# Optimization experiments

Hardware: AMD Instinct MI355X
Metric: run time of the kernel (lower is better)

## Reference

```python
import jax, jax.numpy as jnp
import numpy as np

N = 50000          # nodes
E = 800000         # edges
D_IN = 96          # node_encoding_length
D = 128            # hidden_encoding_length (args.node_encoding)
B = 512            # graphs in batch
MPNN_STEPS = 4
S2S_STEPS = 3


def setup_inputs() -> dict:
    key = jax.random.key(0)
    ks = jax.random.split(key, 12)
    x = jax.random.normal(ks[0], (N, D_IN), dtype=jnp.float32)
    edge_index = jax.random.randint(ks[1], (2, E), 0, N, dtype=jnp.int64)
    batch = jnp.sort(jax.random.randint(ks[2], (N,), 0, B, dtype=jnp.int64))
    s_in = 1.0 / np.sqrt(D_IN)
    W_in = jax.random.uniform(ks[3], (D, D_IN), jnp.float32, -s_in, s_in)
    b_in = jax.random.uniform(ks[4], (D,), jnp.float32, -s_in, s_in)
    s_l = 1.0 / np.sqrt(D)
    W_ih = jax.random.uniform(ks[5], (4 * D, 2 * D), jnp.float32, -s_l, s_l)
    W_hh = jax.random.uniform(ks[6], (4 * D, D), jnp.float32, -s_l, s_l)
    b_ih = jax.random.uniform(ks[7], (4 * D,), jnp.float32, -s_l, s_l)
    b_hh = jax.random.uniform(ks[8], (4 * D,), jnp.float32, -s_l, s_l)
    s_p = 1.0 / np.sqrt(2 * D)
    W_pred = jax.random.uniform(ks[9], (1, 2 * D), jnp.float32, -s_p, s_p)
    b_pred = jax.random.uniform(ks[10], (1,), jnp.float32, -s_p, s_p)
    return {"x": x, "edge_index": edge_index, "batch": batch,
            "W_in": W_in, "b_in": b_in, "W_ih": W_ih, "W_hh": W_hh,
            "b_ih": b_ih, "b_hh": b_hh, "W_pred": W_pred, "b_pred": b_pred}


def _forward(x, edge_index, batch, W_in, b_in, W_ih, W_hh, b_ih, b_hh, W_pred, b_pred):
    # input layer + relu
    h = jax.nn.relu(x @ W_in.T + b_in)                      # [N, D]
    src, dst = edge_index[0], edge_index[1]
    # precompute in-degree for mean aggregation (clamped to 1 like scatter-mean)
    deg = jax.ops.segment_sum(jnp.ones((E,), h.dtype), dst, num_segments=N)
    deg = jnp.maximum(deg, 1.0)[:, None]                    # [N, 1]
    # MPNN: gather x_j at src, mean-aggregate at dst, update x=(x+msg)/2
    for _ in range(MPNN_STEPS):
        msg = jax.ops.segment_sum(h[src], dst, num_segments=N) / deg
        h = (h + msg) * 0.5
    # Set2Set readout
    d = h.shape[1]
    q_star = jnp.zeros((B, 2 * d), h.dtype)
    hh = jnp.zeros((B, d), h.dtype)
    cc = jnp.zeros((B, d), h.dtype)
    for _ in range(S2S_STEPS):
        gates = q_star @ W_ih.T + b_ih + hh @ W_hh.T + b_hh  # [B, 4d]
        i_g, f_g, g_g, o_g = jnp.split(gates, 4, axis=-1)
        cc = jax.nn.sigmoid(f_g) * cc + jax.nn.sigmoid(i_g) * jnp.tanh(g_g)
        hh = jax.nn.sigmoid(o_g) * jnp.tanh(cc)
        q = hh                                               # [B, d]
        e = jnp.sum(h * q[batch], axis=-1)                   # [N]
        e_max = jax.ops.segment_max(e, batch, num_segments=B)
        a = jnp.exp(e - e_max[batch])
        a_sum = jax.ops.segment_sum(a, batch, num_segments=B)
        a = a / (a_sum[batch] + 1e-16)
        r = jax.ops.segment_sum(a[:, None] * h, batch, num_segments=B)  # [B, d]
        q_star = jnp.concatenate([q, r], axis=-1)
    return q_star @ W_pred.T + b_pred                        # [B, 1]


def reference(x, edge_index, batch, W_in, b_in, W_ih, W_hh, b_ih, b_hh, W_pred, b_pred):
    return _forward(x, edge_index, batch, W_in, b_in, W_ih, W_hh, b_ih, b_hh, W_pred, b_pred)
```

## Files before the change

kernel.cpp:

```cpp
#include <hip/hip_runtime.h>
#include <math.h>
#include <float.h>

#define N_NODES 50000
#define N_EDGES 800000
#define D_INP   96
#define D_HID   128
#define N_B     512
#define CAP     64
#define XS_LD   100

typedef __attribute__((ext_vector_type(4))) _Float16 half4;

__global__ void k_prep(const float* __restrict__ W_in,
                       const float* __restrict__ W_ih,
                       const float* __restrict__ W_hh,
                       float* __restrict__ Wt_in,
                       float* __restrict__ Wt2,
                       int* __restrict__ cnt) {
    int idx = blockIdx.x * 256 + threadIdx.x;
    if (idx < N_NODES) cnt[idx] = 0;
    if (idx < D_INP * D_HID) {
        int k = idx / D_HID, d = idx % D_HID;
        Wt_in[idx] = W_in[d * D_INP + k];
    }
    if (idx < 256 * 512) {
        int k = idx / 512, g = idx % 512;
        float v = W_ih[g * 256 + k];
        if (k < 128) v += W_hh[g * 128 + k];
        Wt2[idx] = v;
    }
}

__global__ void k_bucket(const int* __restrict__ src, const int* __restrict__ dst,
                         const int* __restrict__ batch,
                         int* __restrict__ cnt, int* __restrict__ esrc,
                         int* __restrict__ seg_ptr) {
    int e = blockIdx.x * 256 + threadIdx.x;
    if (e < N_EDGES) {
        int d = dst[e];
        int p = atomicAdd(&cnt[d], 1);
        if (p < CAP) esrc[d * CAP + p] = src[e];
    }
    if (e < N_NODES) {
        int n = e;
        int bc = batch[n];
        int bp = (n == 0) ? -1 : batch[n - 1];
        for (int b = bp + 1; b <= bc; b++) seg_ptr[b] = n;
        if (n == N_NODES - 1)
            for (int b = bc + 1; b <= N_B; b++) seg_ptr[b] = N_NODES;
    }
}

__global__ __launch_bounds__(256) void k_ingemm(const float* __restrict__ x,
                                                const float* __restrict__ Wt_in,
                                                const float* __restrict__ b_in,
                                                float* __restrict__ h,
                                                _Float16* __restrict__ h16) {
    __shared__ __align__(16) float xs[64 * XS_LD];
    __shared__ __align__(16) float ws[96 * 64];
    int n0 = blockIdx.x * 64;
    int d0 = blockIdx.y * 64;
    int tid = threadIdx.x;
    for (int j = tid; j < 64 * 96 / 4; j += 256) {
        int row = (j * 4) / 96, col = (j * 4) % 96;
        int node = n0 + row;
        float4 v = make_float4(0.f, 0.f, 0.f, 0.f);
        if (node < N_NODES) v = *(const float4*)&x[(size_t)node * 96 + col];
        *(float4*)&xs[row * XS_LD + col] = v;
    }
    for (int j = tid; j < 96 * 64 / 4; j += 256) {
        int k = (j * 4) / 64, dd = (j * 4) % 64;
        *(float4*)&ws[j * 4] = *(const float4*)&Wt_in[k * D_HID + d0 + dd];
    }
    __syncthreads();
    int tn = tid / 16;
    int td = tid % 16;
    float acc[4][4] = {};
    for (int k0 = 0; k0 < 96; k0 += 4) {
        float4 w0 = *(float4*)&ws[(k0 + 0) * 64 + td * 4];
        float4 w1 = *(float4*)&ws[(k0 + 1) * 64 + td * 4];
        float4 w2 = *(float4*)&ws[(k0 + 2) * 64 + td * 4];
        float4 w3 = *(float4*)&ws[(k0 + 3) * 64 + td * 4];
#pragma unroll
        for (int j = 0; j < 4; j++) {
            float4 xv = *(float4*)&xs[(tn * 4 + j) * XS_LD + k0];
            acc[j][0] += xv.x * w0.x + xv.y * w1.x + xv.z * w2.x + xv.w * w3.x;
            acc[j][1] += xv.x * w0.y + xv.y * w1.y + xv.z * w2.y + xv.w * w3.y;
            acc[j][2] += xv.x * w0.z + xv.y * w1.z + xv.z * w2.z + xv.w * w3.z;
            acc[j][3] += xv.x * w0.w + xv.y * w1.w + xv.z * w2.w + xv.w * w3.w;
        }
    }
    float4 bb = *(const float4*)&b_in[d0 + td * 4];
#pragma unroll
    for (int j = 0; j < 4; j++) {
        int node = n0 + tn * 4 + j;
        if (node < N_NODES) {
            float4 o;
            o.x = fmaxf(acc[j][0] + bb.x, 0.f);
            o.y = fmaxf(acc[j][1] + bb.y, 0.f);
            o.z = fmaxf(acc[j][2] + bb.z, 0.f);
            o.w = fmaxf(acc[j][3] + bb.w, 0.f);
            *(float4*)&h[(size_t)node * D_HID + d0 + td * 4] = o;
            half4 s;
            s.x = (_Float16)o.x; s.y = (_Float16)o.y;
            s.z = (_Float16)o.z; s.w = (_Float16)o.w;
            *(half4*)&h16[(size_t)node * D_HID + d0 + td * 4] = s;
        }
    }
}

template <bool WRITE16>
__global__ __launch_bounds__(256) void k_mpnn(const float* __restrict__ hin,
                                              const _Float16* __restrict__ hin16,
                                              float* __restrict__ hout,
                                              _Float16* __restrict__ hout16,
                                              const int* __restrict__ cnt,
                                              const int* __restrict__ esrc) {
    int g = threadIdx.x >> 5;
    int l = threadIdx.x & 31;
    int n = blockIdx.x * 8 + g;
    if (n >= N_NODES) return;
    int deg = cnt[n];
    int len = min(deg, CAP);
    const int* row = &esrc[n * CAP];
    float4 a0 = {0,0,0,0}, a1 = {0,0,0,0}, a2 = {0,0,0,0}, a3 = {0,0,0,0};
    int i = 0;
    for (; i + 4 <= len; i += 4) {
        int e0 = row[i + 0];
        int e1 = row[i + 1];
        int e2 = row[i + 2];
        int e3 = row[i + 3];
        half4 v0 = *(const half4*)&hin16[(size_t)e0 * 128 + l * 4];
        half4 v1 = *(const half4*)&hin16[(size_t)e1 * 128 + l * 4];
        half4 v2 = *(const half4*)&hin16[(size_t)e2 * 128 + l * 4];
        half4 v3 = *(const half4*)&hin16[(size_t)e3 * 128 + l * 4];
        a0.x += (float)v0.x; a0.y += (float)v0.y; a0.z += (float)v0.z; a0.w += (float)v0.w;
        a1.x += (float)v1.x; a1.y += (float)v1.y; a1.z += (float)v1.z; a1.w += (float)v1.w;
        a2.x += (float)v2.x; a2.y += (float)v2.y; a2.z += (float)v2.z; a2.w += (float)v2.w;
        a3.x += (float)v3.x; a3.y += (float)v3.y; a3.z += (float)v3.z; a3.w += (float)v3.w;
    }
    for (; i < len; i++) {
        int e0 = row[i];
        half4 v0 = *(const half4*)&hin16[(size_t)e0 * 128 + l * 4];
        a0.x += (float)v0.x; a0.y += (float)v0.y; a0.z += (float)v0.z; a0.w += (float)v0.w;
    }
    a0.x += a1.x + a2.x + a3.x;
    a0.y += a1.y + a2.y + a3.y;
    a0.z += a1.z + a2.z + a3.z;
    a0.w += a1.w + a2.w + a3.w;
    float invd = 1.0f / (float)max(deg, 1);
    float4 hv = *(const float4*)&hin[(size_t)n * 128 + l * 4];
    float4 o;
    o.x = (hv.x + a0.x * invd) * 0.5f;
    o.y = (hv.y + a0.y * invd) * 0.5f;
    o.z = (hv.z + a0.z * invd) * 0.5f;
    o.w = (hv.w + a0.w * invd) * 0.5f;
    *(float4*)&hout[(size_t)n * 128 + l * 4] = o;
    if (WRITE16) {
        half4 s;
        s.x = (_Float16)o.x; s.y = (_Float16)o.y;
        s.z = (_Float16)o.z; s.w = (_Float16)o.w;
        *(half4*)&hout16[(size_t)n * 128 + l * 4] = s;
    }
}

__device__ __forceinline__ float sigmoidf_(float v) { return 1.0f / (1.0f + expf(-v)); }

__global__ __launch_bounds__(1024) void k_s2s2(const float* __restrict__ Wt2,
                                               const float* __restrict__ b_ih,
                                               const float* __restrict__ b_hh,
                                               const float* __restrict__ h,
                                               const int* __restrict__ seg_ptr,
                                               const float* __restrict__ W_pred,
                                               const float* __restrict__ b_pred,
                                               float* __restrict__ out) {
    __shared__ __align__(16) float in_s[2 * 256];
    __shared__ __align__(16) float c_s[2 * 128];
    __shared__ __align__(16) float gates_s[2 * 512];
    __shared__ __align__(16) float gpart_s[2][2][512];
    __shared__ float smax_s[2][16];
    __shared__ float ssum_s[2][16];
    __shared__ __align__(16) float sr_s[2][16][128];

    int t = threadIdx.x;
    if (t < 512) in_s[t] = 0.f;
    if (t < 256) c_s[t] = 0.f;

    int gate = t & 511;
    int kh   = t >> 9;
    int row  = t >> 9;
    int loc  = t & 511;
    int gq   = loc >> 5;
    int l    = t & 31;
    int b    = blockIdx.x * 2 + row;
    int s0 = seg_ptr[b], s1 = seg_ptr[b + 1];

    for (int step = 0; step < 3; step++) {
        __syncthreads();
        {
            float acc0 = 0.f, acc1 = 0.f;
            int k0 = kh * 128;
#pragma unroll 8
            for (int k = k0; k < k0 + 128; k++) {
                float w = Wt2[k * 512 + gate];
                acc0 += in_s[k] * w;
                acc1 += in_s[256 + k] * w;
            }
            gpart_s[kh][0][gate] = acc0;
            gpart_s[kh][1][gate] = acc1;
        }
        __syncthreads();
        if (t < 512) {
            float bia = b_ih[t] + b_hh[t];
            gates_s[t]       = gpart_s[0][0][t] + gpart_s[1][0][t] + bia;
            gates_s[512 + t] = gpart_s[0][1][t] + gpart_s[1][1][t] + bia;
        }
        __syncthreads();
        if (t < 256) {
            int r2 = t >> 7, ff = t & 127;
            float ig = gates_s[r2 * 512 + ff];
            float fg = gates_s[r2 * 512 + 128 + ff];
            float gg = gates_s[r2 * 512 + 256 + ff];
            float og = gates_s[r2 * 512 + 384 + ff];
            float c = sigmoidf_(fg) * c_s[r2 * 128 + ff] + sigmoidf_(ig) * tanhf(gg);
            c_s[r2 * 128 + ff] = c;
            in_s[r2 * 256 + ff] = sigmoidf_(og) * tanhf(c);
        }
        __syncthreads();
        float4 q = *(float4*)&in_s[row * 256 + l * 4];
        float Ma = -INFINITY, sa = 0.f;
        float Mb = -INFINITY, sb = 0.f;
        float4 ra = make_float4(0.f, 0.f, 0.f, 0.f);
        float4 rb = make_float4(0.f, 0.f, 0.f, 0.f);
        for (int n = s0 + gq; n < s1; n += 32) {
            {
                float4 hv = *(const float4*)&h[(size_t)n * 128 + l * 4];
                float d = hv.x * q.x + hv.y * q.y + hv.z * q.z + hv.w * q.w;
                for (int m = 16; m >= 1; m >>= 1) d += __shfl_xor(d, m, 64);
                float nM = fmaxf(Ma, d);
                float sc = expf(Ma - nM);
                float a = expf(d - nM);
                sa = sa * sc + a;
                ra.x = ra.x * sc + a * hv.x;
                ra.y = ra.y * sc + a * hv.y;
                ra.z = ra.z * sc + a * hv.z;
                ra.w = ra.w * sc + a * hv.w;
                Ma = nM;
            }
            int n2 = n + 16;
            if (n2 < s1) {
                float4 hv = *(const float4*)&h[(size_t)n2 * 128 + l * 4];
                float d = hv.x * q.x + hv.y * q.y + hv.z * q.z + hv.w * q.w;
                for (int m = 16; m >= 1; m >>= 1) d += __shfl_xor(d, m, 64);
                float nM = fmaxf(Mb, d);
                float sc = expf(Mb - nM);
                float a = expf(d - nM);
                sb = sb * sc + a;
                rb.x = rb.x * sc + a * hv.x;
                rb.y = rb.y * sc + a * hv.y;
                rb.z = rb.z * sc + a * hv.z;
                rb.w = rb.w * sc + a * hv.w;
                Mb = nM;
            }
        }
        float M = fmaxf(Ma, Mb);
        float wa = (Ma > -INFINITY) ? expf(Ma - M) : 0.f;
        float wb = (Mb > -INFINITY) ? expf(Mb - M) : 0.f;
        float asum = sa * wa + sb * wb;
        float4 racc;
        racc.x = ra.x * wa + rb.x * wb;
        racc.y = ra.y * wa + rb.y * wb;
        racc.z = ra.z * wa + rb.z * wb;
        racc.w = ra.w * wa + rb.w * wb;
        if (l == 0) { smax_s[row][gq] = M; ssum_s[row][gq] = asum; }
        *(float4*)&sr_s[row][gq][l * 4] = racc;
        __syncthreads();
        if (gq == 0) {
            float Mx = -INFINITY;
#pragma unroll
            for (int i = 0; i < 16; i++) Mx = fmaxf(Mx, smax_s[row][i]);
            float4 o = make_float4(0.f, 0.f, 0.f, 0.f);
            if (Mx > -INFINITY) {
                float tot = 0.f;
                float4 osum = make_float4(0.f, 0.f, 0.f, 0.f);
#pragma unroll
                for (int i = 0; i < 16; i++) {
                    float wi = expf(smax_s[row][i] - Mx);
                    tot += ssum_s[row][i] * wi;
                    float4 ri = *(float4*)&sr_s[row][i][l * 4];
                    osum.x += ri.x * wi; osum.y += ri.y * wi;
                    osum.z += ri.z * wi; osum.w += ri.w * wi;
                }
                float inv = 1.0f / (tot + 1e-16f);
                o.x = osum.x * inv; o.y = osum.y * inv;
                o.z = osum.z * inv; o.w = osum.w * inv;
            }
            *(float4*)&in_s[row * 256 + 128 + l * 4] = o;
            if (step == 2) {
                float4 wq = *(const float4*)&W_pred[l * 4];
                float4 wr = *(const float4*)&W_pred[128 + l * 4];
                float d = q.x * wq.x + q.y * wq.y + q.z * wq.z + q.w * wq.w
                        + o.x * wr.x + o.y * wr.y + o.z * wr.z + o.w * wr.w;
                for (int m = 16; m >= 1; m >>= 1) d += __shfl_xor(d, m, 64);
                if (l == 0) out[b] = d + b_pred[0];
            }
        }
    }
}

extern "C" void kernel_launch(void* const* d_in, const int* in_sizes, int n_in,
                              void* d_out, int out_size, void* d_ws, size_t ws_size,
                              hipStream_t stream) {
    const float* x      = (const float*)d_in[0];
    const int*   edge   = (const int*)d_in[1];
    const int*   batch  = (const int*)d_in[2];
    const float* W_in   = (const float*)d_in[3];
    const float* b_in   = (const float*)d_in[4];
    const float* W_ih   = (const float*)d_in[5];
    const float* W_hh   = (const float*)d_in[6];
    const float* b_ih   = (const float*)d_in[7];
    const float* b_hh   = (const float*)d_in[8];
    const float* W_pred = (const float*)d_in[9];
    const float* b_pred = (const float*)d_in[10];
    float* out = (float*)d_out;

    const int* src = edge;
    const int* dst = edge + N_EDGES;

    float* f = (float*)d_ws;
    float* h0    = f;                     f += (size_t)N_NODES * D_HID;
    float* h1    = f;                     f += (size_t)N_NODES * D_HID;
    _Float16* g0 = (_Float16*)f;          f += (size_t)N_NODES * D_HID / 2;
    _Float16* g1 = (_Float16*)f;          f += (size_t)N_NODES * D_HID / 2;
    float* Wt_in = f;                     f += D_INP * D_HID;
    float* Wt2   = f;                     f += 256 * 512;
    int* ip = (int*)f;
    int* cnt     = ip;                    ip += N_NODES;
    int* seg_ptr = ip;                    ip += N_B + 1 + 3;
    int* esrc    = ip;                    ip += (size_t)N_NODES * CAP;

    k_prep<<<768, 256, 0, stream>>>(W_in, W_ih, W_hh, Wt_in, Wt2, cnt);

    k_bucket<<<(N_EDGES + 255) / 256, 256, 0, stream>>>(src, dst, batch,
                                                        cnt, esrc, seg_ptr);

    k_ingemm<<<dim3((N_NODES + 63) / 64, 2), 256, 0, stream>>>(x, Wt_in, b_in, h0, g0);

    int mb = (N_NODES + 7) / 8;
    k_mpnn<true ><<<mb, 256, 0, stream>>>(h0, g0, h1, g1, cnt, esrc);
    k_mpnn<true ><<<mb, 256, 0, stream>>>(h1, g1, h0, g0, cnt, esrc);
    k_mpnn<true ><<<mb, 256, 0, stream>>>(h0, g0, h1, g1, cnt, esrc);
    k_mpnn<false><<<mb, 256, 0, stream>>>(h1, g1, h0, g0, cnt, esrc);

    k_s2s2<<<N_B / 2, 1024, 0, stream>>>(Wt2, b_ih, b_hh, h0, seg_ptr,
                                         W_pred, b_pred, out);
}
```

Baseline: 346.3 us.

## Use 16-bit edge indices, half8 gathers, and fp16 hidden state for readout

Edge source indices are stored as unsigned short instead of int, which halves the bucket-list footprint. N=50000 fits in 16 bits. The MPNN kernel now uses 16 lanes per node with 8-wide half loads and handles 16 nodes per block. The last MPNN step writes only the fp16 copy, and the Set2Set readout reads h in fp16 instead of fp32, which cuts the bandwidth of the attention passes. The trade is lower precision in the readout's dot products and weighted sums.

Result: faster. 337.6 us (-2.5%).

```diff
diff --git a/kernel.cpp b/kernel.cpp
--- a/kernel.cpp
+++ b/kernel.cpp
@@ -11,6 +11,7 @@
 #define XS_LD   100
 
 typedef __attribute__((ext_vector_type(4))) _Float16 half4;
+typedef __attribute__((ext_vector_type(8))) _Float16 half8;
 
 __global__ void k_prep(const float* __restrict__ W_in,
                        const float* __restrict__ W_ih,
@@ -34,13 +35,13 @@
 
 __global__ void k_bucket(const int* __restrict__ src, const int* __restrict__ dst,
                          const int* __restrict__ batch,
-                         int* __restrict__ cnt, int* __restrict__ esrc,
+                         int* __restrict__ cnt, unsigned short* __restrict__ esrc,
                          int* __restrict__ seg_ptr) {
     int e = blockIdx.x * 256 + threadIdx.x;
     if (e < N_EDGES) {
         int d = dst[e];
         int p = atomicAdd(&cnt[d], 1);
-        if (p < CAP) esrc[d * CAP + p] = src[e];
+        if (p < CAP) esrc[(size_t)d * CAP + p] = (unsigned short)src[e];
     }
     if (e < N_NODES) {
         int n = e;
@@ -110,59 +111,69 @@
     }
 }
 
-template <bool WRITE16>
+template <bool WRITE32>
 __global__ __launch_bounds__(256) void k_mpnn(const float* __restrict__ hin,
                                               const _Float16* __restrict__ hin16,
                                               float* __restrict__ hout,
                                               _Float16* __restrict__ hout16,
                                               const int* __restrict__ cnt,
-                                              const int* __restrict__ esrc) {
-    int g = threadIdx.x >> 5;
-    int l = threadIdx.x & 31;
-    int n = blockIdx.x * 8 + g;
+                                              const unsigned short* __restrict__ esrc) {
+    int g = threadIdx.x >> 4;
+    int l = threadIdx.x & 15;
+    int n = blockIdx.x * 16 + g;
     if (n >= N_NODES) return;
     int deg = cnt[n];
     int len = min(deg, CAP);
-    const int* row = &esrc[n * CAP];
-    float4 a0 = {0,0,0,0}, a1 = {0,0,0,0}, a2 = {0,0,0,0}, a3 = {0,0,0,0};
+    const unsigned short* row = &esrc[(size_t)n * CAP];
+    float a0[8] = {}, a1[8] = {}, a2[8] = {}, a3[8] = {};
     int i = 0;
     for (; i + 4 <= len; i += 4) {
         int e0 = row[i + 0];
         int e1 = row[i + 1];
         int e2 = row[i + 2];
         int e3 = row[i + 3];
-        half4 v0 = *(const half4*)&hin16[(size_t)e0 * 128 + l * 4];
-        half4 v1 = *(const half4*)&hin16[(size_t)e1 * 128 + l * 4];
-        half4 v2 = *(const half4*)&hin16[(size_t)e2 * 128 + l * 4];
-        half4 v3 = *(const half4*)&hin16[(size_t)e3 * 128 + l * 4];
-        a0.x += (float)v0.x; a0.y += (float)v0.y; a0.z += (float)v0.z; a0.w += (float)v0.w;
-        a1.x += (float)v1.x; a1.y += (float)v1.y; a1.z += (float)v1.z; a1.w += (float)v1.w;
-        a2.x += (float)v2.x; a2.y += (float)v2.y; a2.z += (float)v2.z; a2.w += (float)v2.w;
-        a3.x += (float)v3.x; a3.y += (float)v3.y; a3.z += (float)v3.z; a3.w += (float)v3.w;
+        half8 v0 = *(const half8*)&hin16[(size_t)e0 * 128 + l * 8];
+        half8 v1 = *(const half8*)&hin16[(size_t)e1 * 128 + l * 8];
+        half8 v2 = *(const half8*)&hin16[(size_t)e2 * 128 + l * 8];
+        half8 v3 = *(const half8*)&hin16[(size_t)e3 * 128 + l * 8];
+#pragma unroll
+        for (int c = 0; c < 8; c++) {
+            a0[c] += (float)v0[c];
+            a1[c] += (float)v1[c];
+            a2[c] += (float)v2[c];
+            a3[c] += (float)v3[c];
+        }
     }
     for (; i < len; i++) {
         int e0 = row[i];
-        half4 v0 = *(const half4*)&hin16[(size_t)e0 * 128 + l * 4];
-        a0.x += (float)v0.x; a0.y += (float)v0.y; a0.z += (float)v0.z; a0.w += (float)v0.w;
-    }
-    a0.x += a1.x + a2.x + a3.x;
-    a0.y += a1.y + a2.y + a3.y;
-    a0.z += a1.z + a2.z + a3.z;
-    a0.w += a1.w + a2.w + a3.w;
+        half8 v0 = *(const half8*)&hin16[(size_t)e0 * 128 + l * 8];
+#pragma unroll
+        for (int c = 0; c < 8; c++) a0[c] += (float)v0[c];
+    }
+#pragma unroll
+    for (int c = 0; c < 8; c++) a0[c] += a1[c] + a2[c] + a3[c];
     float invd = 1.0f / (float)max(deg, 1);
-    float4 hv = *(const float4*)&hin[(size_t)n * 128 + l * 4];
-    float4 o;
-    o.x = (hv.x + a0.x * invd) * 0.5f;
-    o.y = (hv.y + a0.y * invd) * 0.5f;
-    o.z = (hv.z + a0.z * invd) * 0.5f;
-    o.w = (hv.w + a0.w * invd) * 0.5f;
-    *(float4*)&hout[(size_t)n * 128 + l * 4] = o;
-    if (WRITE16) {
-        half4 s;
-        s.x = (_Float16)o.x; s.y = (_Float16)o.y;
-        s.z = (_Float16)o.z; s.w = (_Float16)o.w;
-        *(half4*)&hout16[(size_t)n * 128 + l * 4] = s;
-    }
+    float4 s0 = *(const float4*)&hin[(size_t)n * 128 + l * 8];
+    float4 s1 = *(const float4*)&hin[(size_t)n * 128 + l * 8 + 4];
+    float o[8];
+    o[0] = (s0.x + a0[0] * invd) * 0.5f;
+    o[1] = (s0.y + a0[1] * invd) * 0.5f;
+    o[2] = (s0.z + a0[2] * invd) * 0.5f;
+    o[3] = (s0.w + a0[3] * invd) * 0.5f;
+    o[4] = (s1.x + a0[4] * invd) * 0.5f;
+    o[5] = (s1.y + a0[5] * invd) * 0.5f;
+    o[6] = (s1.z + a0[6] * invd) * 0.5f;
+    o[7] = (s1.w + a0[7] * invd) * 0.5f;
+    if (WRITE32) {
+        float4 w0 = make_float4(o[0], o[1], o[2], o[3]);
+        float4 w1 = make_float4(o[4], o[5], o[6], o[7]);
+        *(float4*)&hout[(size_t)n * 128 + l * 8] = w0;
+        *(float4*)&hout[(size_t)n * 128 + l * 8 + 4] = w1;
+    }
+    half8 s;
+#pragma unroll
+    for (int c = 0; c < 8; c++) s[c] = (_Float16)o[c];
+    *(half8*)&hout16[(size_t)n * 128 + l * 8] = s;
 }
 
 __device__ __forceinline__ float sigmoidf_(float v) { return 1.0f / (1.0f + expf(-v)); }
@@ -170,7 +181,7 @@
 __global__ __launch_bounds__(1024) void k_s2s2(const float* __restrict__ Wt2,
                                                const float* __restrict__ b_ih,
                                                const float* __restrict__ b_hh,
-                                               const float* __restrict__ h,
+                                               const _Float16* __restrict__ h16,
                                                const int* __restrict__ seg_ptr,
                                                const float* __restrict__ W_pred,
                                                const float* __restrict__ b_pred,
@@ -235,7 +246,8 @@
         float4 rb = make_float4(0.f, 0.f, 0.f, 0.f);
         for (int n = s0 + gq; n < s1; n += 32) {
             {
-                float4 hv = *(const float4*)&h[(size_t)n * 128 + l * 4];
+                half4 h4 = *(const half4*)&h16[(size_t)n * 128 + l * 4];
+                float4 hv = make_float4((float)h4.x, (float)h4.y, (float)h4.z, (float)h4.w);
                 float d = hv.x * q.x + hv.y * q.y + hv.z * q.z + hv.w * q.w;
                 for (int m = 16; m >= 1; m >>= 1) d += __shfl_xor(d, m, 64);
                 float nM = fmaxf(Ma, d);
@@ -250,7 +262,8 @@
             }
             int n2 = n + 16;
             if (n2 < s1) {
-                float4 hv = *(const float4*)&h[(size_t)n2 * 128 + l * 4];
+                half4 h4 = *(const half4*)&h16[(size_t)n2 * 128 + l * 4];
+                float4 hv = make_float4((float)h4.x, (float)h4.y, (float)h4.z, (float)h4.w);
                 float d = hv.x * q.x + hv.y * q.y + hv.z * q.z + hv.w * q.w;
                 for (int m = 16; m >= 1; m >>= 1) d += __shfl_xor(d, m, 64);
                 float nM = fmaxf(Mb, d);
@@ -338,7 +351,7 @@
     int* ip = (int*)f;
     int* cnt     = ip;                    ip += N_NODES;
     int* seg_ptr = ip;                    ip += N_B + 1 + 3;
-    int* esrc    = ip;                    ip += (size_t)N_NODES * CAP;
+    unsigned short* esrc = (unsigned short*)ip;
 
     k_prep<<<768, 256, 0, stream>>>(W_in, W_ih, W_hh, Wt_in, Wt2, cnt);
 
@@ -347,12 +360,12 @@
 
     k_ingemm<<<dim3((N_NODES + 63) / 64, 2), 256, 0, stream>>>(x, Wt_in, b_in, h0, g0);
 
-    int mb = (N_NODES + 7) / 8;
+    int mb = (N_NODES + 15) / 16;
     k_mpnn<true ><<<mb, 256, 0, stream>>>(h0, g0, h1, g1, cnt, esrc);
     k_mpnn<true ><<<mb, 256, 0, stream>>>(h1, g1, h0, g0, cnt, esrc);
     k_mpnn<true ><<<mb, 256, 0, stream>>>(h0, g0, h1, g1, cnt, esrc);
     k_mpnn<false><<<mb, 256, 0, stream>>>(h1, g1, h0, g0, cnt, esrc);
 
-    k_s2s2<<<N_B / 2, 1024, 0, stream>>>(Wt2, b_ih, b_hh, h0, seg_ptr,
+    k_s2s2<<<N_B / 2, 1024, 0, stream>>>(Wt2, b_ih, b_hh, g0, seg_ptr,
                                          W_pred, b_pred, out);
 }
```
